# Kernel tuning notes

Measured on AMD Instinct MI355X. Metric: run time of the kernel, lower is better.

## Reference

```python
import jax, jax.numpy as jnp
import numpy as np
from jax import lax

NPOINT = 1024
K = 32
EPS = 1e-5  # BatchNorm2d default eps


def setup_inputs() -> dict:
    key = jax.random.key(0)
    ks = jax.random.split(key, 8)
    B, N = 16, 4096
    xyz = jax.random.normal(ks[0], (B, N, 3), dtype=jnp.float32)
    init_farthest = jax.random.randint(ks[1], (B,), 0, N, dtype=jnp.int32)
    def w(k, o, i):
        return jax.random.normal(k, (o, i), dtype=jnp.float32) * (1.0 / np.sqrt(i))
    chans = [3, 64, 64, 128]
    inp = {"xyz": xyz, "init_farthest": init_farthest}
    for li in range(3):
        ci, co = chans[li], chans[li + 1]
        inp[f"W{li+1}"] = w(ks[2 + li], co, ci)
        inp[f"b{li+1}"] = jnp.zeros((co,), jnp.float32)
        inp[f"g{li+1}"] = jnp.ones((co,), jnp.float32)
        inp[f"be{li+1}"] = jnp.zeros((co,), jnp.float32)
    return inp


def _farthest_point_sample(xyz, init_farthest, npoint):
    # Sequential FPS: npoint iterations of distance-update + argmax (lax.scan).
    B, N, _ = xyz.shape
    bidx = jnp.arange(B)
    def step(carry, _):
        distance, farthest = carry
        centroid = xyz[bidx, farthest][:, None, :]            # [B,1,3]
        d = jnp.sum((xyz - centroid) ** 2, axis=-1)           # [B,N]
        distance = jnp.minimum(distance, d)
        return (distance, jnp.argmax(distance, axis=-1)), farthest
    init = (jnp.full((B, N), 1e10, xyz.dtype), init_farthest)
    _, centroids = lax.scan(step, init, None, length=npoint)  # [npoint,B]
    return centroids.T                                        # [B,npoint]


def _forward(xyz, init_farthest, params):
    B, N, _ = xyz.shape
    fps_idx = _farthest_point_sample(xyz, init_farthest, NPOINT)      # [B,S]
    bidx = jnp.arange(B)[:, None]
    new_xyz = xyz[bidx, fps_idx]                                       # [B,S,3]
    # KNN over sampled points (pairwise squared distances, [B,S,S])
    dist = jnp.sum((new_xyz[:, :, None, :] - new_xyz[:, None, :, :]) ** 2, axis=-1)
    idx = jnp.argsort(dist, axis=-1)[:, :, 1:K + 1]                    # [B,S,K]
    # NOTE: faithful to original code: idx (values < npoint) indexes xyz rows.
    grouped = xyz[jnp.arange(B)[:, None, None], idx]                   # [B,S,K,3]
    grouped = grouped - new_xyz[:, :, None, :]
    x = jnp.transpose(grouped, (0, 3, 1, 2))                           # [B,3,S,K]
    for (W, b, g, be) in params:
        x = jnp.einsum('oc,bcsk->bosk', W, x) + b[None, :, None, None]
        m = x.mean(axis=(0, 2, 3), keepdims=True)
        v = x.var(axis=(0, 2, 3), keepdims=True)                       # biased var (BN train mode)
        x = g[None, :, None, None] * (x - m) * lax.rsqrt(v + EPS) + be[None, :, None, None]
        x = jax.nn.relu(x)
    new_points = jnp.max(x, axis=-1)                                   # [B,128,S]
    return new_xyz, new_points


def reference(xyz, init_farthest, W1, b1, g1, be1, W2, b2, g2, be2, W3, b3, g3, be3):
    params = [(W1, b1, g1, be1), (W2, b2, g2, be2), (W3, b3, g3, be3)]
    return _forward(xyz, init_farthest, params)
```

## Files before the change

### kernel.cpp

```cpp
#include <hip/hip_runtime.h>


#define Bc 16
#define Nn 4096
#define Ss 1024
#define Kk 32
#define COLS (Bc*Ss*Kk)
#define EPSF 1e-5f

#define S2SUM 16
#define S2SQ  528
#define S3SUM 1040
#define S3SQ  2064

typedef unsigned long long ull;
typedef unsigned int uint32;
typedef __attribute__((ext_vector_type(8))) short bf16x8;
typedef __attribute__((ext_vector_type(4))) float f32x4;

__device__ __forceinline__ unsigned short f2bf(float f){
  uint32 u = __float_as_uint(f);
  uint32 r = (u + 0x7fffu + ((u>>16)&1u)) >> 16;
  return (unsigned short)r;
}
__device__ __forceinline__ float bf2f(unsigned short h){ return __uint_as_float(((uint32)h)<<16); }

__device__ __forceinline__ float dppmax_f32(float x){
  #define STEPF(ctrl,rm) { int _s=__builtin_amdgcn_update_dpp(__float_as_int(x),__float_as_int(x),(ctrl),(rm),0xf,false); x=fmaxf(x,__int_as_float(_s)); }
  STEPF(0x111,0xf) STEPF(0x112,0xf) STEPF(0x114,0xf) STEPF(0x118,0xf)
  STEPF(0x142,0xa) STEPF(0x143,0xc)
  #undef STEPF
  return __int_as_float(__builtin_amdgcn_readlane(__float_as_int(x),63));
}
__device__ __forceinline__ int dppmin_i32(int x){
  #define STEPI(ctrl,rm) { int _s=__builtin_amdgcn_update_dpp(x,x,(ctrl),(rm),0xf,false); x=min(x,_s); }
  STEPI(0x111,0xf) STEPI(0x112,0xf) STEPI(0x114,0xf) STEPI(0x118,0xf)
  STEPI(0x142,0xa) STEPI(0x143,0xc)
  #undef STEPI
  return __builtin_amdgcn_readlane(x,63);
}
__device__ __forceinline__ float dpprowsum(float x){
  #define SSTEP(ctrl) { int _s=__builtin_amdgcn_update_dpp(__float_as_int(x),__float_as_int(x),(ctrl),0xf,0xf,false); x+=__int_as_float(_s); }
  SSTEP(0x111) SSTEP(0x112) SSTEP(0x114) SSTEP(0x118)
  #undef SSTEP
  return x;
}

__global__ __launch_bounds__(256) void fps_kernel(const float* __restrict__ xyz,
                                                  const int* __restrict__ init_far,
                                                  float* __restrict__ new_xyz){
  __shared__ float sx[Nn*4];
  __shared__ ull wk[2][4];
  int b = blockIdx.x, t = threadIdx.x;
  int lane = t & 63, wid = t >> 6;
  const float* xb = xyz + (size_t)b*Nn*3;
  const float4* xb4 = (const float4*)xb;
  for(int i=t;i<Nn*3/4;i+=256){
    float4 v = xb4[i];
    int f0 = 4*i;
    sx[(f0/3)*4 + (f0%3)]       = v.x;
    sx[((f0+1)/3)*4 + ((f0+1)%3)] = v.y;
    sx[((f0+2)/3)*4 + ((f0+2)%3)] = v.z;
    sx[((f0+3)/3)*4 + ((f0+3)%3)] = v.w;
  }
  __syncthreads();
  const float4* sxp = (const float4*)sx;
  float px[16],py[16],pz[16],dd[16];
  #pragma unroll
  for(int j=0;j<16;j++){ int n=t+256*j; float4 p=sxp[n]; px[j]=p.x; py[j]=p.y; pz[j]=p.z; dd[j]=1e10f; }
  int far = init_far[b];
  float o0x=0.f,o0y=0.f,o0z=0.f, o1x=0.f,o1y=0.f,o1z=0.f;
  float o2x=0.f,o2y=0.f,o2z=0.f, o3x=0.f,o3y=0.f,o3z=0.f;
  for(int it=0; it<Ss; it++){
    float4 c4 = sxp[far];
    float cx=c4.x, cy=c4.y, cz=c4.z;
    if(t==(it&255)){
      if(it<256)      { o0x=cx; o0y=cy; o0z=cz; }
      else if(it<512) { o1x=cx; o1y=cy; o1z=cz; }
      else if(it<768) { o2x=cx; o2y=cy; o2z=cz; }
      else            { o3x=cx; o3y=cy; o3z=cz; }
    }
    #pragma unroll
    for(int j=0;j<16;j++){
      float dx=px[j]-cx, dy=py[j]-cy, dz=pz[j]-cz;
      float d=__fadd_rn(__fadd_rn(__fmul_rn(dx,dx),__fmul_rn(dy,dy)),__fmul_rn(dz,dz));
      dd[j]=fminf(dd[j],d);
    }
    float m0=fmaxf(fmaxf(fmaxf(dd[0],dd[1]),fmaxf(dd[2],dd[3])),fmaxf(fmaxf(dd[4],dd[5]),fmaxf(dd[6],dd[7])));
    float m1=fmaxf(fmaxf(fmaxf(dd[8],dd[9]),fmaxf(dd[10],dd[11])),fmaxf(fmaxf(dd[12],dd[13]),fmaxf(dd[14],dd[15])));
    float bd=fmaxf(m0,m1);
    float dmax = dppmax_f32(bd);
    int cj=16;
    #pragma unroll
    for(int j=15;j>=0;j--) cj = (dd[j]!=dmax) ? cj : j;
    int cand = t + (cj<<8);
    int wmin = dppmin_i32(cand);
    if(lane==0) wk[it&1][wid] = ((ull)__float_as_uint(dmax)<<32) | (uint32)(4095-wmin);
    __syncthreads();
    ull g0=wk[it&1][0], g1=wk[it&1][1], g2=wk[it&1][2], g3=wk[it&1][3];
    ull ka = g1>g0?g1:g0, kb = g3>g2?g3:g2;
    ull kg = kb>ka?kb:ka;
    far = 4095-(int)(uint32)(kg&0xffffffffu);
  }
  float* outb = new_xyz + (size_t)b*Ss*3;
  outb[t*3+0]=o0x; outb[t*3+1]=o0y; outb[t*3+2]=o0z;
  outb[(256+t)*3+0]=o1x; outb[(256+t)*3+1]=o1y; outb[(256+t)*3+2]=o1z;
  outb[(512+t)*3+0]=o2x; outb[(512+t)*3+1]=o2y; outb[(512+t)*3+2]=o2z;
  outb[(768+t)*3+0]=o3x; outb[(768+t)*3+1]=o3y; outb[(768+t)*3+2]=o3z;
}

#define KN16(X) X(0) X(1) X(2) X(3) X(4) X(5) X(6) X(7) X(8) X(9) X(10) X(11) X(12) X(13) X(14) X(15)

__global__ __launch_bounds__(256) void knn_kernel(const float* __restrict__ xyz,
                                                  const float* __restrict__ new_xyz,
                                                  float* __restrict__ gout){
  __shared__ float nx[Ss*3];
  int b = blockIdx.x >> 8;
  int t = threadIdx.x;
  const float4* src=(const float4*)(new_xyz + (size_t)b*Ss*3);
  float4* dst=(float4*)nx;
  for(int i=t;i<Ss*3/4;i+=256) dst[i]=src[i];
  __syncthreads();
  int wid=t>>6, lane=t&63;
  int s=(blockIdx.x&255)*4+wid;
  float qx=nx[s*3],qy=nx[s*3+1],qz=nx[s*3+2];
  #define KDECL(i) ull K##i;
  KN16(KDECL)
  #undef KDECL
  #define KINIT(i) { int j=lane+64*(i); \
    float dx=nx[j*3]-qx, dy=nx[j*3+1]-qy, dz=nx[j*3+2]-qz; \
    float d=__fadd_rn(__fadd_rn(__fmul_rn(dx,dx),__fmul_rn(dy,dy)),__fmul_rn(dz,dz)); \
    K##i=((ull)(__float_as_uint(d)+1u)<<32)|(uint32)(j); }
  KN16(KINIT)
  #undef KINIT
  ull last=0; int myn=0;
  for(int r=0;r<33;r++){
    ull cur=~0ull;
    #define KSCAN(i) { ull c=K##i; c=(c>last)?c:~0ull; cur=(c<cur)?c:cur; }
    KN16(KSCAN)
    #undef KSCAN
    int hs=(int)(uint32)(cur>>32);
    hs = (hs<0) ? 0x7fffffff : hs;
    int dmin = dppmin_i32(hs);
    int ci = (hs==dmin) ? (int)(uint32)cur : 0x7fffffff;
    int jmin = dppmin_i32(ci);
    last = ((ull)(uint32)dmin<<32)|(uint32)jmin;
    if(r>=1 && lane==r-1) myn=jmin;
  }
  if(lane<Kk){
    int j=myn;
    const float* p=xyz + (size_t)b*Nn*3 + (size_t)j*3;
    float* go = gout + ((size_t)(b*Ss+s)*Kk + lane)*3;
    go[0]=p[0]-qx; go[1]=p[1]-qy; go[2]=p[2]-qz;
  }
}

__global__ __launch_bounds__(256) void gmom_kernel(const float* __restrict__ g, float* __restrict__ stats){
  __shared__ float sm[9];
  int t=threadIdx.x;
  if(t<9) sm[t]=0.f;
  __syncthreads();
  float a[9]={0,0,0,0,0,0,0,0,0};
  for(int col=blockIdx.x*256+t; col<COLS; col+=gridDim.x*256){
    float x=g[(size_t)col*3],y=g[(size_t)col*3+1],z=g[(size_t)col*3+2];
    a[0]+=x;a[1]+=y;a[2]+=z;a[3]+=x*x;a[4]+=y*y;a[5]+=z*z;a[6]+=x*y;a[7]+=x*z;a[8]+=y*z;
  }
  #pragma unroll
  for(int i=0;i<9;i++){
    float v=a[i];
    #pragma unroll
    for(int m=32;m>=1;m>>=1) v+=__shfl_xor(v,m,64);
    if((t&63)==0) atomicAdd(&sm[i],v);
  }
  __syncthreads();
  if(t<9) atomicAdd(&stats[t],sm[t]);
}

__global__ __launch_bounds__(256) void layer12_kernel(const float* __restrict__ g,
    const float* __restrict__ W1,const float* __restrict__ b1,const float* __restrict__ g1,const float* __restrict__ be1,
    const float* __restrict__ W2,const float* __restrict__ b2,
    const float* __restrict__ stats, unsigned short* __restrict__ y2,
    float* __restrict__ statsw){
  __shared__ unsigned short x2s[128*72];
  __shared__ unsigned short w2b[64*72];
  __shared__ float w1s[192], b1s[64], sc1[64], sh1[64], b2s[64];
  __shared__ float rs2[64], rq2[64];
  int t=threadIdx.x;
  for(int i=t;i<4096;i+=256) w2b[(i>>6)*72+(i&63)]=f2bf(W2[i]);
  if(t<192) w1s[t]=W1[t];
  if(t<64){ b1s[t]=b1[t]; b2s[t]=b2[t]; rs2[t]=0.f; rq2[t]=0.f; }
  __syncthreads();
  if(t<64){
    const float n1=1.0f/COLS;
    float ex=stats[0]*n1,ey=stats[1]*n1,ez=stats[2]*n1;
    float cxx=stats[3]*n1-ex*ex, cyy=stats[4]*n1-ey*ey, czz=stats[5]*n1-ez*ez;
    float cxy=stats[6]*n1-ex*ey, cxz=stats[7]*n1-ex*ez, cyz=stats[8]*n1-ey*ez;
    float wx=w1s[t*3],wy=w1s[t*3+1],wz=w1s[t*3+2];
    float m=wx*ex+wy*ey+wz*ez+b1s[t];
    float v=wx*wx*cxx+wy*wy*cyy+wz*wz*czz+2.f*(wx*wy*cxy+wx*wz*cxz+wy*wz*cyz);
    float sc=g1[t]*rsqrtf(v+EPSF);
    sc1[t]=sc; sh1[t]=be1[t]-m*sc;
  }
  __syncthreads();
  {
    int col=t&127, c0=(t>>7)*32;
    size_t cg=(size_t)blockIdx.x*128+col;
    float gx=g[cg*3],gy=g[cg*3+1],gz=g[cg*3+2];
    uint32 ou[16];
    #pragma unroll
    for(int ci=0;ci<16;ci++){
      int c=c0+2*ci;
      float ya=fmaf(w1s[c*3],gx,fmaf(w1s[c*3+1],gy,fmaf(w1s[c*3+2],gz,b1s[c])));
      float va=fmaxf(fmaf(ya,sc1[c],sh1[c]),0.f);
      float yb=fmaf(w1s[c*3+3],gx,fmaf(w1s[c*3+4],gy,fmaf(w1s[c*3+5],gz,b1s[c+1])));
      float vb=fmaxf(fmaf(yb,sc1[c+1],sh1[c+1]),0.f);
      ou[ci]=(uint32)f2bf(va) | ((uint32)f2bf(vb)<<16);
    }
    uint32* xu=(uint32*)x2s;
    #pragma unroll
    for(int h=0;h<4;h++){
      ((uint4*)(xu + col*36 + (c0>>1)))[h] = make_uint4(ou[h*4],ou[h*4+1],ou[h*4+2],ou[h*4+3]);
    }
  }
  __syncthreads();
  int w=t>>6, lane=t&63, quad=lane>>4, lr=lane&15;
  f32x4 acc[4][2];
  #pragma unroll
  for(int mt=0;mt<4;mt++){ acc[mt][0]=(f32x4){0.f,0.f,0.f,0.f}; acc[mt][1]=(f32x4){0.f,0.f,0.f,0.f}; }
  #pragma unroll
  for(int kt=0;kt<2;kt++){
    int ko=kt*32+quad*8;
    bf16x8 b0=*(const bf16x8*)&x2s[(w*32+lr)*72+ko];
    bf16x8 b1v=*(const bf16x8*)&x2s[(w*32+16+lr)*72+ko];
    #pragma unroll
    for(int mt=0;mt<4;mt++){
      bf16x8 a=*(const bf16x8*)&w2b[(mt*16+lr)*72+ko];
      acc[mt][0]=__builtin_amdgcn_mfma_f32_16x16x32_bf16(a,b0,acc[mt][0],0,0,0);
      acc[mt][1]=__builtin_amdgcn_mfma_f32_16x16x32_bf16(a,b1v,acc[mt][1],0,0,0);
    }
  }
  size_t col0=(size_t)blockIdx.x*128 + w*32 + lr;
  #pragma unroll
  for(int mt=0;mt<4;mt++){
    ushort4 p0,p1;
    unsigned short* q0=(unsigned short*)&p0;
    unsigned short* q1=(unsigned short*)&p1;
    #pragma unroll
    for(int r=0;r<4;r++){
      int o=mt*16+quad*4+r;
      float bb=b2s[o];
      float v0=acc[mt][0][r]+bb, v1=acc[mt][1][r]+bb;
      q0[r]=f2bf(v0); q1[r]=f2bf(v1);
      float s_=v0+v1, sq_=fmaf(v0,v0,v1*v1);
      s_=dpprowsum(s_); sq_=dpprowsum(sq_);
      if(lr==15){ atomicAdd(&rs2[o],s_); atomicAdd(&rq2[o],sq_); }
    }
    *(ushort4*)(y2 + col0*64 + mt*16+quad*4) = p0;
    *(ushort4*)(y2 + (col0+16)*64 + mt*16+quad*4) = p1;
  }
  __syncthreads();
  if(t<64){
    int rep=blockIdx.x&7;
    atomicAdd(&statsw[S2SUM+rep*64+t],rs2[t]);
    atomicAdd(&statsw[S2SQ +rep*64+t],rq2[t]);
  }
}

__global__ __launch_bounds__(256) void layer3_kernel(const unsigned short* __restrict__ y2,
    const float* __restrict__ g2,const float* __restrict__ be2,
    const float* __restrict__ W3,const float* __restrict__ b3,
    float* __restrict__ stats, float* __restrict__ ymax, float* __restrict__ ymin){
  __shared__ unsigned short x3s[64*72];
  __shared__ unsigned short w3b[128*72];
  __shared__ float y3s[128*65];
  __shared__ float sc2[64], sh2[64], b3s[128];
  int t=threadIdx.x;
  if(t<64){
    const float n1=1.0f/COLS;
    float ssum=0.f, ssq=0.f;
    #pragma unroll
    for(int rp=0;rp<8;rp++){ ssum+=stats[S2SUM+rp*64+t]; ssq+=stats[S2SQ+rp*64+t]; }
    float m=ssum*n1;
    float v=ssq*n1-m*m;
    float sc=g2[t]*rsqrtf(v+EPSF);
    sc2[t]=sc; sh2[t]=be2[t]-m*sc;
  }
  if(t<128) b3s[t]=b3[t];
  for(int i=t;i<8192;i+=256) w3b[(i>>6)*72+(i&63)]=f2bf(W3[i]);
  __syncthreads();
  int w=t>>6, lane=t&63, quad=lane>>4, lr=lane&15;
  int q=t>>7, oo=t&127;
  float asum=0.f, asq=0.f;
  for(int tl=0; tl<4; tl++){
    int colbase=(blockIdx.x*4+tl)*64;
    {
      int col=t&63, c0=(t>>6)*16;
      const unsigned short* yp=y2+(size_t)(colbase+col)*64+c0;
      uint32 ou[8];
      #pragma unroll
      for(int h=0;h<2;h++){
        uint4 u=((const uint4*)yp)[h];
        uint32 ua[4]={u.x,u.y,u.z,u.w};
        #pragma unroll
        for(int e=0;e<4;e++){
          int c=c0+h*8+e*2;
          float flo=__uint_as_float(ua[e]<<16);
          float fhi=__uint_as_float(ua[e]&0xffff0000u);
          float v0=fmaxf(fmaf(flo,sc2[c],sh2[c]),0.f);
          float v1=fmaxf(fmaf(fhi,sc2[c+1],sh2[c+1]),0.f);
          ou[h*4+e]=(uint32)f2bf(v0) | ((uint32)f2bf(v1)<<16);
        }
      }
      uint32* xu=(uint32*)x3s;
      #pragma unroll
      for(int h=0;h<2;h++){
        ((uint4*)(xu + col*36 + (c0>>1)))[h] = make_uint4(ou[h*4],ou[h*4+1],ou[h*4+2],ou[h*4+3]);
      }
    }
    __syncthreads();
    f32x4 acc[8];
    #pragma unroll
    for(int mt=0;mt<8;mt++) acc[mt]=(f32x4){0.f,0.f,0.f,0.f};
    #pragma unroll
    for(int kt=0;kt<2;kt++){
      int ko=kt*32+quad*8;
      bf16x8 bfr=*(const bf16x8*)&x3s[(w*16+lr)*72+ko];
      #pragma unroll
      for(int mt=0;mt<8;mt++){
        bf16x8 afr=*(const bf16x8*)&w3b[(mt*16+lr)*72+ko];
        acc[mt]=__builtin_amdgcn_mfma_f32_16x16x32_bf16(afr,bfr,acc[mt],0,0,0);
      }
    }
    #pragma unroll
    for(int mt=0;mt<8;mt++){
      #pragma unroll
      for(int r=0;r<4;r++){
        int o=mt*16+quad*4+r;
        y3s[o*65 + w*16+lr]=acc[mt][r]+b3s[o];
      }
    }
    __syncthreads();
    {
      float mx=-3.4e38f, mn=3.4e38f, su=0.f, sq=0.f;
      #pragma unroll
      for(int k=0;k<32;k++){
        float yv=y3s[oo*65+q*32+k];
        mx=fmaxf(mx,yv); mn=fminf(mn,yv); su+=yv; sq=fmaf(yv,yv,sq);
      }
      asum+=su; asq+=sq;
      int qg=(colbase>>5)+q;
      int bb=qg>>10, ss=qg&1023;
      ymax[((size_t)bb*128+oo)*1024+ss]=mx;
      ymin[((size_t)bb*128+oo)*1024+ss]=mn;
    }
    __syncthreads();
  }
  if(t>=128){ y3s[t-128]=asum; y3s[128+(t-128)]=asq; }
  __syncthreads();
  if(t<128){
    asum+=y3s[t]; asq+=y3s[128+t];
    int rep=blockIdx.x&7;
    atomicAdd(&stats[S3SUM+rep*128+t],asum);
    atomicAdd(&stats[S3SQ +rep*128+t],asq);
  }
}

__global__ __launch_bounds__(256) void finalize_kernel(const float* __restrict__ ymax,const float* __restrict__ ymin,
    const float* __restrict__ g3,const float* __restrict__ be3,const float* __restrict__ stats,
    float* __restrict__ outp){
  int idx=blockIdx.x*256+threadIdx.x;
  int o=(idx>>10)&127;
  const float n1=1.0f/COLS;
  float ssum=0.f, ssq=0.f;
  #pragma unroll
  for(int rp=0;rp<8;rp++){ ssum+=stats[S3SUM+rp*128+o]; ssq+=stats[S3SQ+rp*128+o]; }
  float m=ssum*n1;
  float v=ssq*n1-m*m;
  float sc=g3[o]*rsqrtf(v+EPSF);
  float sh=be3[o]-m*sc;
  float val=(sc>=0.f)?ymax[idx]:ymin[idx];
  outp[idx]=fmaxf(fmaf(val,sc,sh),0.f);
}

extern "C" void kernel_launch(void* const* d_in, const int* in_sizes, int n_in,
                              void* d_out, int out_size, void* d_ws, size_t ws_size,
                              hipStream_t stream){
  const float* xyz=(const float*)d_in[0];
  const int* initf=(const int*)d_in[1];
  const float* W1=(const float*)d_in[2]; const float* b1=(const float*)d_in[3];
  const float* g1=(const float*)d_in[4]; const float* be1=(const float*)d_in[5];
  const float* W2=(const float*)d_in[6]; const float* b2=(const float*)d_in[7];
  const float* g2=(const float*)d_in[8]; const float* be2=(const float*)d_in[9];
  const float* W3=(const float*)d_in[10]; const float* b3=(const float*)d_in[11];
  const float* g3=(const float*)d_in[12]; const float* be3=(const float*)d_in[13];
  float* out=(float*)d_out;
  char* ws=(char*)d_ws;
  float* stats=(float*)(ws);
  float* gbuf=(float*)(ws+65536);
  unsigned short* y2=(unsigned short*)(ws+6361088);
  float* ymax=(float*)(ws+73469952);
  float* ymin=(float*)(ws+81858560);
  hipMemsetAsync(stats,0,16384,stream);
  fps_kernel<<<16,256,0,stream>>>(xyz,initf,out);
  knn_kernel<<<4096,256,0,stream>>>(xyz,out,gbuf);
  gmom_kernel<<<1024,256,0,stream>>>(gbuf,stats);
  layer12_kernel<<<4096,256,0,stream>>>(gbuf,W1,b1,g1,be1,W2,b2,stats,y2,stats);
  layer3_kernel<<<2048,256,0,stream>>>(y2,g2,be2,W3,b3,stats,ymax,ymin);
  finalize_kernel<<<8192,256,0,stream>>>(ymax,ymin,g3,be3,stats,out+49152);
}
```

Baseline: 982.3 us.

## Replace FPS barrier with tagged spin-wait and fuse moment stats into KNN

The FPS loop no longer calls __syncthreads each iteration. Each wave publishes a packed key tagged with the iteration number into LDS and spins on volatile reads until all four waves' tags match, which removes the block barrier from the 1024-step sequential loop. The separate gmom kernel is removed: the KNN kernel computes the nine first and second moments of the grouped offsets with a DPP wave reduction and atomically adds them into eight spread slots, which layer12 then sums. This relies on LDS visibility between waves without a fence, and the spin has a bounded retry count as a safety valve.

```diff
diff --git a/kernel.cpp b/kernel.cpp
--- a/kernel.cpp
+++ b/kernel.cpp
@@ -12,6 +12,7 @@
 #define S2SQ  528
 #define S3SUM 1040
 #define S3SQ  2064
+#define GM    3328
 
 typedef unsigned long long ull;
 typedef unsigned int uint32;
@@ -43,6 +44,13 @@
   #define SSTEP(ctrl) { int _s=__builtin_amdgcn_update_dpp(__float_as_int(x),__float_as_int(x),(ctrl),0xf,0xf,false); x+=__int_as_float(_s); }
   SSTEP(0x111) SSTEP(0x112) SSTEP(0x114) SSTEP(0x118)
   #undef SSTEP
+  return x;
+}
+__device__ __forceinline__ float dppsum64(float x){
+  #define ASTEP(ctrl,rm) { int _s=__builtin_amdgcn_update_dpp(0,__float_as_int(x),(ctrl),(rm),0xf,false); x+=__int_as_float(_s); }
+  ASTEP(0x111,0xf) ASTEP(0x112,0xf) ASTEP(0x114,0xf) ASTEP(0x118,0xf)
+  ASTEP(0x142,0xa) ASTEP(0x143,0xc)
+  #undef ASTEP
   return x;
 }
 
@@ -63,6 +71,7 @@
     sx[((f0+2)/3)*4 + ((f0+2)%3)] = v.z;
     sx[((f0+3)/3)*4 + ((f0+3)%3)] = v.w;
   }
+  if(t<8) ((ull*)wk)[t]=0ull;
   __syncthreads();
   const float4* sxp = (const float4*)sx;
   float px[16],py[16],pz[16],dd[16];
@@ -95,12 +104,18 @@
     for(int j=15;j>=0;j--) cj = (dd[j]!=dmax) ? cj : j;
     int cand = t + (cj<<8);
     int wmin = dppmin_i32(cand);
-    if(lane==0) wk[it&1][wid] = ((ull)__float_as_uint(dmax)<<32) | (uint32)(4095-wmin);
-    __syncthreads();
-    ull g0=wk[it&1][0], g1=wk[it&1][1], g2=wk[it&1][2], g3=wk[it&1][3];
+    uint32 tag = (uint32)(it+1)<<12;
+    volatile ull* wv = wk[it&1];
+    if(lane==0) wk[it&1][wid] = ((ull)__float_as_uint(dmax)<<32) | tag | (uint32)(4095-wmin);
+    ull g0,g1,g2,g3;
+    int tries=0;
+    do{
+      g0=wv[0]; g1=wv[1]; g2=wv[2]; g3=wv[3];
+    }while((((((uint32)g0)^tag)|(((uint32)g1)^tag)|(((uint32)g2)^tag)|(((uint32)g3)^tag)) & 0xFFFFF000u)
+           && ++tries<1000000);
     ull ka = g1>g0?g1:g0, kb = g3>g2?g3:g2;
     ull kg = kb>ka?kb:ka;
-    far = 4095-(int)(uint32)(kg&0xffffffffu);
+    far = 4095-(int)((uint32)kg & 0xFFFu);
   }
   float* outb = new_xyz + (size_t)b*Ss*3;
   outb[t*3+0]=o0x; outb[t*3+1]=o0y; outb[t*3+2]=o0z;
@@ -113,13 +128,16 @@
 
 __global__ __launch_bounds__(256) void knn_kernel(const float* __restrict__ xyz,
                                                   const float* __restrict__ new_xyz,
-                                                  float* __restrict__ gout){
+                                                  float* __restrict__ gout,
+                                                  float* __restrict__ stats){
   __shared__ float nx[Ss*3];
+  __shared__ float sm[9];
   int b = blockIdx.x >> 8;
   int t = threadIdx.x;
   const float4* src=(const float4*)(new_xyz + (size_t)b*Ss*3);
   float4* dst=(float4*)nx;
   for(int i=t;i<Ss*3/4;i+=256) dst[i]=src[i];
+  if(t<9) sm[t]=0.f;
   __syncthreads();
   int wid=t>>6, lane=t&63;
   int s=(blockIdx.x&255)*4+wid;
@@ -147,33 +165,22 @@
     last = ((ull)(uint32)dmin<<32)|(uint32)jmin;
     if(r>=1 && lane==r-1) myn=jmin;
   }
+  float gx=0.f,gy=0.f,gz=0.f;
   if(lane<Kk){
     int j=myn;
     const float* p=xyz + (size_t)b*Nn*3 + (size_t)j*3;
+    gx=p[0]-qx; gy=p[1]-qy; gz=p[2]-qz;
     float* go = gout + ((size_t)(b*Ss+s)*Kk + lane)*3;
-    go[0]=p[0]-qx; go[1]=p[1]-qy; go[2]=p[2]-qz;
-  }
-}
-
-__global__ __launch_bounds__(256) void gmom_kernel(const float* __restrict__ g, float* __restrict__ stats){
-  __shared__ float sm[9];
-  int t=threadIdx.x;
-  if(t<9) sm[t]=0.f;
-  __syncthreads();
-  float a[9]={0,0,0,0,0,0,0,0,0};
-  for(int col=blockIdx.x*256+t; col<COLS; col+=gridDim.x*256){
-    float x=g[(size_t)col*3],y=g[(size_t)col*3+1],z=g[(size_t)col*3+2];
-    a[0]+=x;a[1]+=y;a[2]+=z;a[3]+=x*x;a[4]+=y*y;a[5]+=z*z;a[6]+=x*y;a[7]+=x*z;a[8]+=y*z;
-  }
+    go[0]=gx; go[1]=gy; go[2]=gz;
+  }
+  float a[9]={gx,gy,gz,gx*gx,gy*gy,gz*gz,gx*gy,gx*gz,gy*gz};
   #pragma unroll
   for(int i=0;i<9;i++){
-    float v=a[i];
-    #pragma unroll
-    for(int m=32;m>=1;m>>=1) v+=__shfl_xor(v,m,64);
-    if((t&63)==0) atomicAdd(&sm[i],v);
-  }
-  __syncthreads();
-  if(t<9) atomicAdd(&stats[t],sm[t]);
+    float v=dppsum64(a[i]);
+    if(lane==63) atomicAdd(&sm[i],v);
+  }
+  __syncthreads();
+  if(t<9) atomicAdd(&stats[GM+(blockIdx.x&7)*16+t],sm[t]);
 }
 
 __global__ __launch_bounds__(256) void layer12_kernel(const float* __restrict__ g,
@@ -192,9 +199,17 @@
   __syncthreads();
   if(t<64){
     const float n1=1.0f/COLS;
-    float ex=stats[0]*n1,ey=stats[1]*n1,ez=stats[2]*n1;
-    float cxx=stats[3]*n1-ex*ex, cyy=stats[4]*n1-ey*ey, czz=stats[5]*n1-ez*ez;
-    float cxy=stats[6]*n1-ex*ey, cxz=stats[7]*n1-ex*ez, cyz=stats[8]*n1-ey*ez;
+    float mo[9];
+    #pragma unroll
+    for(int i=0;i<9;i++){
+      float a=0.f;
+      #pragma unroll
+      for(int rp=0;rp<8;rp++) a+=stats[GM+rp*16+i];
+      mo[i]=a;
+    }
+    float ex=mo[0]*n1,ey=mo[1]*n1,ez=mo[2]*n1;
+    float cxx=mo[3]*n1-ex*ex, cyy=mo[4]*n1-ey*ey, czz=mo[5]*n1-ez*ez;
+    float cxy=mo[6]*n1-ex*ey, cxz=mo[7]*n1-ex*ez, cyz=mo[8]*n1-ey*ez;
     float wx=w1s[t*3],wy=w1s[t*3+1],wz=w1s[t*3+2];
     float m=wx*ex+wy*ey+wz*ez+b1s[t];
     float v=wx*wx*cxx+wy*wy*cyy+wz*wz*czz+2.f*(wx*wy*cxy+wx*wz*cxz+wy*wz*cyz);
@@ -402,8 +417,7 @@
   float* ymin=(float*)(ws+81858560);
   hipMemsetAsync(stats,0,16384,stream);
   fps_kernel<<<16,256,0,stream>>>(xyz,initf,out);
-  knn_kernel<<<4096,256,0,stream>>>(xyz,out,gbuf);
-  gmom_kernel<<<1024,256,0,stream>>>(gbuf,stats);
+  knn_kernel<<<4096,256,0,stream>>>(xyz,out,gbuf,stats);
   layer12_kernel<<<4096,256,0,stream>>>(gbuf,W1,b1,g1,be1,W2,b2,stats,y2,stats);
   layer3_kernel<<<2048,256,0,stream>>>(y2,g2,be2,W3,b3,stats,ymax,ymin);
   finalize_kernel<<<8192,256,0,stream>>>(ymax,ymin,g3,be3,stats,out+49152);
```

Result: slower. 1.068 ms (+8.7%).
